# Kernel tuning notes

Hardware: AMD Instinct MI355X
Metric: run time of the kernel (lower is better)

## Reference

```python
import jax, jax.numpy as jnp
import numpy as np

MAX_REL = 128  # max_relative_position


def setup_inputs() -> dict:
    key = jax.random.key(0)
    k1, k2, k3, k4 = jax.random.split(key, 4)
    B, H, S, D = 2, 8, 2048, 64
    q = jax.random.normal(k1, (B, H, S, D), dtype=jnp.float32)
    k = jax.random.normal(k2, (B, H, S, D), dtype=jnp.float32)
    v = jax.random.normal(k3, (B, H, S, D), dtype=jnp.float32)
    rel_table = jax.random.normal(k4, (2 * MAX_REL + 1, D), dtype=jnp.float32)
    return {"q": q, "k": k, "v": v, "rel_table": rel_table}


def reference(q, k, v, rel_table):
    B, H, S, D = q.shape
    scale = jnp.sqrt(jnp.asarray(D, q.dtype))
    # content scores: [B,H,S,S]
    qk_scores = jnp.einsum('bhqd,bhkd->bhqk', q, k)
    # relative position index matrix [S,S] clamped to [-MAX_REL, MAX_REL]
    pos = jnp.arange(S)
    rel_idx = jnp.clip(pos[None, :] - pos[:, None], -MAX_REL, MAX_REL) + MAX_REL
    rel_emb = rel_table[rel_idx]  # [S,S,D]
    # relative scores: per-query dot with rel embedding row -> [B,H,S,S]
    rel_scores = jnp.einsum('bhqd,qkd->bhqk', q, rel_emb)
    scores = (qk_scores + rel_scores) / scale
    attn = jax.nn.softmax(scores, axis=-1)
    # output: [B,H,S,D]
    return jnp.einsum('bhqk,bhkd->bhqd', attn, v)
```

## Files before the change

### kernel.cpp

```cpp
#include <hip/hip_runtime.h>

typedef _Float16 half8 __attribute__((ext_vector_type(8)));
typedef _Float16 half4 __attribute__((ext_vector_type(4)));
typedef float f32x4 __attribute__((ext_vector_type(4)));

#define S_LEN 2048
#define HDIM 64
#define QBLK 64
#define KVBLK 64
#define NT (S_LEN / KVBLK)
#define QRS 258
#define NBH 16
#define L2E 1.44269504f
#define TSTR 72

__device__ __forceinline__ void load_lds16(const void* g, void* l) {
    __builtin_amdgcn_global_load_lds(
        (const __attribute__((address_space(1))) unsigned int*)g,
        (__attribute__((address_space(3))) unsigned int*)l, 16, 0, 0);
}

__global__ __launch_bounds__(256)
void convert_kv_kernel(const float* __restrict__ Kg, const float* __restrict__ Vg,
                       _Float16* __restrict__ Kh, _Float16* __restrict__ Vp)
{
    __shared__ _Float16 tile[KVBLK * TSTR];
    const int bid = blockIdx.x;
    const int tid = threadIdx.x;
    if (bid < 1024) {
        const int id = bid * 256 + tid;
        const int r  = id >> 3;
        const int d0 = (id & 7) * 8;
        const float* src = Kg + (size_t)r * HDIM + d0;
        f32x4 f0 = *(const f32x4*)(src);
        f32x4 f1 = *(const f32x4*)(src + 4);
        half8 h;
#pragma unroll
        for (int j = 0; j < 4; ++j) { h[j] = (_Float16)f0[j]; h[j+4] = (_Float16)f1[j]; }
        const int bh = r >> 11, kvg = r & 2047;
        const int t = kvg >> 6, kv = kvg & 63;
        const size_t blk = (size_t)(bh * NT + t) * 8192;
        const int off = (kv * 128 + d0 * 2) ^ ((kv & 7) << 4);
        *(half8*)((char*)Kh + blk + off) = h;
    } else {
        const int bt = bid - 1024;
        const int bh = bt >> 5, t = bt & 31;
        {
            const int kv = tid >> 2;
            const int d0 = (tid & 3) * 16;
            const float* src = Vg + ((size_t)bh * S_LEN + t * KVBLK + kv) * HDIM + d0;
            f32x4 f0 = *(const f32x4*)(src);
            f32x4 f1 = *(const f32x4*)(src + 4);
            f32x4 f2 = *(const f32x4*)(src + 8);
            f32x4 f3 = *(const f32x4*)(src + 12);
            half8 h0, h1;
#pragma unroll
            for (int j = 0; j < 4; ++j) {
                h0[j] = (_Float16)f0[j]; h0[j+4] = (_Float16)f1[j];
                h1[j] = (_Float16)f2[j]; h1[j+4] = (_Float16)f3[j];
            }
            *(half8*)&tile[kv * TSTR + d0]     = h0;
            *(half8*)&tile[kv * TSTR + d0 + 8] = h1;
        }
        __syncthreads();
        {
            const int dp = tid >> 2;
            const int u0 = (tid & 3) * 2;
            char* base = (char*)Vp + (size_t)bt * 8192;
            const int dsw = (dp & 7) << 4;
#pragma unroll
            for (int ui = 0; ui < 2; ++ui) {
                const int u  = u0 + ui;
                const int kc = u >> 2, gg = u & 3;
                half8 ch;
#pragma unroll
                for (int r = 0; r < 4; ++r) {
                    ch[r]     = tile[(32*kc + 4*gg + r)      * TSTR + dp];
                    ch[4 + r] = tile[(32*kc + 16 + 4*gg + r) * TSTR + dp];
                }
                *(half8*)(base + ((dp * 128 + u * 16) ^ dsw)) = ch;
            }
        }
    }
}

__global__ __launch_bounds__(512, 4)
void relattn_v7(const float* __restrict__ Qg, const float* __restrict__ RELg,
                const _Float16* __restrict__ Kh, const _Float16* __restrict__ Vp,
                float* __restrict__ Og)
{
    __shared__ __attribute__((aligned(16))) _Float16 Kbuf[2][4096];
    __shared__ __attribute__((aligned(16))) _Float16 Vbuf[2][4096];
    __shared__ __attribute__((aligned(16))) _Float16 Qrel[QBLK * QRS];
    __shared__ float MLds[2][64];
    __shared__ float LLds[2][64];

    const int tid  = threadIdx.x;
    const int wave = tid >> 6;
    const int lane = tid & 63;
    const int c  = lane & 15;
    const int g  = lane >> 4;
    const int qs = wave & 3;
    const int ks = wave >> 2;

    const int wk = ((blockIdx.x & 7) << 6) + (blockIdx.x >> 3);
    const int bh = wk >> 5;
    const int q0 = (wk & 31) * QBLK;
    const size_t hoff = (size_t)bh * S_LEN * HDIM;

    const int qb0 = q0 + 16 * qs;
    half8 bq[2];
#pragma unroll
    for (int kc = 0; kc < 2; ++kc) {
        const float* src = Qg + hoff + (size_t)(qb0 + c) * HDIM + kc * 32 + g * 8;
        f32x4 f0 = *(const f32x4*)(src);
        f32x4 f1 = *(const f32x4*)(src + 4);
        half8 h;
#pragma unroll
        for (int j = 0; j < 4; ++j) {
            h[j]     = (_Float16)(f0[j] * 0.125f);
            h[j + 4] = (_Float16)(f1[j] * 0.125f);
        }
        bq[kc] = h;
    }

    if (ks == 0) {
#pragma unroll 1
        for (int t = 0; t < 17; ++t) {
            f32x4 acc = {0.f, 0.f, 0.f, 0.f};
            int r = t * 16 + c;
            if (r > 256) r = 256;
#pragma unroll
            for (int kc = 0; kc < 2; ++kc) {
                const float* src = RELg + (size_t)r * HDIM + kc * 32 + g * 8;
                f32x4 f0 = *(const f32x4*)(src);
                f32x4 f1 = *(const f32x4*)(src + 4);
                half8 b;
#pragma unroll
                for (int j = 0; j < 4; ++j) { b[j] = (_Float16)f0[j]; b[j+4] = (_Float16)f1[j]; }
                acc = __builtin_amdgcn_mfma_f32_16x16x32_f16(bq[kc], b, acc, 0, 0, 0);
            }
            const int col = t * 16 + c;
            if (col <= 256) {
#pragma unroll
                for (int reg = 0; reg < 4; ++reg)
                    Qrel[(16 * qs + 4 * g + reg) * QRS + col] = (_Float16)acc[reg];
            }
        }
    }

    const char* kimg = (const char*)Kh + (size_t)bh * NT * 8192;
    const char* vimg = (const char*)Vp + (size_t)bh * NT * 8192;
    load_lds16(kimg + tid * 16, (char*)Kbuf + tid * 16);
    load_lds16(vimg + tid * 16, (char*)Vbuf + tid * 16);

    __syncthreads();

    const _Float16* qr = &Qrel[(16 * qs + c) * QRS];
    const float bias_lo = (float)qr[0];
    const float bias_hi = (float)qr[256];

    const int swz = (c & 7) << 4;
    int akoff[2][2], voff[4];
#pragma unroll
    for (int n = 0; n < 2; ++n)
#pragma unroll
        for (int kc = 0; kc < 2; ++kc)
            akoff[n][kc] = (((32 * ks + 16 * n + c) * 128) + kc * 64 + g * 16) ^ swz;
#pragma unroll
    for (int dn = 0; dn < 4; ++dn)
        voff[dn] = (((16 * dn + c) * 128) + ks * 64 + g * 16) ^ swz;

    half8 ones;
#pragma unroll
    for (int j = 0; j < 8; ++j) ones[j] = (_Float16)1.0f;

    float m = -1e30f;
    f32x4 l_acc = {0.f, 0.f, 0.f, 0.f};
    f32x4 oacc[4];
#pragma unroll
    for (int i = 0; i < 4; ++i) oacc[i] = (f32x4){0.f, 0.f, 0.f, 0.f};

#define BODY(t, b) do {                                                              \
        asm volatile("s_waitcnt vmcnt(0)" ::: "memory");                             \
        __builtin_amdgcn_s_barrier();                                                \
        {                                                                            \
            const int tn = ((t) + 1 < NT) ? (t) + 1 : (t);                           \
            load_lds16(kimg + (size_t)tn * 8192 + tid * 16,                          \
                       (char*)Kbuf + ((b) ^ 1) * 8192 + tid * 16);                   \
            load_lds16(vimg + (size_t)tn * 8192 + tid * 16,                          \
                       (char*)Vbuf + ((b) ^ 1) * 8192 + tid * 16);                   \
        }                                                                            \
        const char* kb = (const char*)Kbuf + (b) * 8192;                             \
        const char* vb = (const char*)Vbuf + (b) * 8192;                             \
        const int kws = (t) * KVBLK + 32 * ks;                                       \
        half8 a00 = *(const half8*)(kb + akoff[0][0]);                               \
        half8 a01 = *(const half8*)(kb + akoff[0][1]);                               \
        half8 a10 = *(const half8*)(kb + akoff[1][0]);                               \
        half8 a11 = *(const half8*)(kb + akoff[1][1]);                               \
        f32x4 s0 = {0.f,0.f,0.f,0.f}, s1 = {0.f,0.f,0.f,0.f};                        \
        __builtin_amdgcn_s_setprio(1);                                               \
        s0 = __builtin_amdgcn_mfma_f32_16x16x32_f16(a00, bq[0], s0, 0, 0, 0);        \
        s1 = __builtin_amdgcn_mfma_f32_16x16x32_f16(a10, bq[0], s1, 0, 0, 0);        \
        s0 = __builtin_amdgcn_mfma_f32_16x16x32_f16(a01, bq[1], s0, 0, 0, 0);        \
        s1 = __builtin_amdgcn_mfma_f32_16x16x32_f16(a11, bq[1], s1, 0, 0, 0);        \
        __builtin_amdgcn_s_setprio(0);                                               \
        float bias = 0.f;                                                            \
        float lm;                                                                    \
        if (kws + 159 <= qb0) {                                                      \
            bias = bias_lo;                                                          \
            lm = fmaxf(fmaxf(fmaxf(s0[0], s0[1]), fmaxf(s0[2], s0[3])),              \
                       fmaxf(fmaxf(s1[0], s1[1]), fmaxf(s1[2], s1[3]))) + bias;      \
        } else if (kws >= qb0 + 143) {                                               \
            bias = bias_hi;                                                          \
            lm = fmaxf(fmaxf(fmaxf(s0[0], s0[1]), fmaxf(s0[2], s0[3])),              \
                       fmaxf(fmaxf(s1[0], s1[1]), fmaxf(s1[2], s1[3]))) + bias;      \
        } else {                                                                     \
            const int base_d = kws + 4 * g - (qb0 + c) + 128;                        \
            _Pragma("unroll")                                                        \
            for (int r = 0; r < 4; ++r) {                                            \
                int i0 = base_d + r;                                                 \
                i0 = i0 < 0 ? 0 : (i0 > 256 ? 256 : i0);                             \
                int i1 = base_d + 16 + r;                                            \
                i1 = i1 < 0 ? 0 : (i1 > 256 ? 256 : i1);                             \
                s0[r] += (float)qr[i0];                                              \
                s1[r] += (float)qr[i1];                                              \
            }                                                                        \
            lm = fmaxf(fmaxf(fmaxf(s0[0], s0[1]), fmaxf(s0[2], s0[3])),              \
                       fmaxf(fmaxf(s1[0], s1[1]), fmaxf(s1[2], s1[3])));             \
        }                                                                            \
        if (!__all(lm <= m + 8.f)) {                                                 \
            float mt = lm;                                                           \
            mt = fmaxf(mt, __shfl_xor(mt, 16, 64));                                  \
            mt = fmaxf(mt, __shfl_xor(mt, 32, 64));                                  \
            const float mnew = fmaxf(m, mt);                                         \
            const float al = __builtin_amdgcn_exp2f((m - mnew) * L2E);               \
            m = mnew;                                                                \
            _Pragma("unroll")                                                        \
            for (int r = 0; r < 4; ++r) {                                            \
                const float ar = __shfl(al, 20 * g + r, 64);                         \
                l_acc[r] *= ar;                                                      \
                _Pragma("unroll")                                                    \
                for (int dn = 0; dn < 4; ++dn) oacc[dn][r] *= ar;                    \
            }                                                                        \
        }                                                                            \
        const float fold = (bias - m) * L2E;                                         \
        half8 ap;                                                                    \
        _Pragma("unroll")                                                            \
        for (int r = 0; r < 4; ++r) {                                                \
            ap[r]     = (_Float16)__builtin_amdgcn_exp2f(fmaf(s0[r], L2E, fold));    \
            ap[4 + r] = (_Float16)__builtin_amdgcn_exp2f(fmaf(s1[r], L2E, fold));    \
        }                                                                            \
        half8 v0 = *(const half8*)(vb + voff[0]);                                    \
        half8 v1 = *(const half8*)(vb + voff[1]);                                    \
        half8 v2 = *(const half8*)(vb + voff[2]);                                    \
        half8 v3 = *(const half8*)(vb + voff[3]);                                    \
        __builtin_amdgcn_s_setprio(1);                                               \
        l_acc   = __builtin_amdgcn_mfma_f32_16x16x32_f16(ap, ones, l_acc, 0, 0, 0);  \
        oacc[0] = __builtin_amdgcn_mfma_f32_16x16x32_f16(ap, v0, oacc[0], 0, 0, 0);  \
        oacc[1] = __builtin_amdgcn_mfma_f32_16x16x32_f16(ap, v1, oacc[1], 0, 0, 0);  \
        oacc[2] = __builtin_amdgcn_mfma_f32_16x16x32_f16(ap, v2, oacc[2], 0, 0, 0);  \
        oacc[3] = __builtin_amdgcn_mfma_f32_16x16x32_f16(ap, v3, oacc[3], 0, 0, 0);  \
        __builtin_amdgcn_s_setprio(0);                                               \
    } while (0)

#pragma unroll 1
    for (int tt = 0; tt < NT; tt += 2) {
        BODY(tt, 0);
        BODY(tt + 1, 1);
    }
#undef BODY

    asm volatile("s_waitcnt vmcnt(0)" ::: "memory");
    __syncthreads();

    {
        char* Ob = (char*)Kbuf;
#pragma unroll
        for (int r = 0; r < 4; ++r) {
            const int row = 16 * qs + 4 * g + r;
            const int rsw = (row & 7) << 4;
#pragma unroll
            for (int dn = 0; dn < 4; ++dn)
                *(_Float16*)(Ob + ks * 8192 + ((row * 128 + (16 * dn + c) * 2) ^ rsw))
                    = (_Float16)oacc[dn][r];
        }
        if (g == 0) MLds[ks][16 * qs + c] = m;
        if (c == 0) {
#pragma unroll
            for (int r = 0; r < 4; ++r)
                LLds[ks][16 * qs + 4 * g + r] = l_acc[r];
        }
        __syncthreads();

        const int row = 16 * qs + c;
        const int rsw = (c & 7) << 4;
        const float m0 = MLds[0][row], m1 = MLds[1][row];
        const float l0 = LLds[0][row], l1 = LLds[1][row];
        const float M  = fmaxf(m0, m1);
        const float w0 = __builtin_amdgcn_exp2f((m0 - M) * L2E);
        const float w1 = __builtin_amdgcn_exp2f((m1 - M) * L2E);
        const float inv = 1.0f / (l0 * w0 + l1 * w1);

        const int dof = 64 * ks + 16 * g;
        half8 o0 = *(const half8*)(Ob +        ((row * 128 + dof) ^ rsw));
        half8 o1 = *(const half8*)(Ob + 8192 + ((row * 128 + dof) ^ rsw));
        float* dst = Og + hoff + (size_t)(q0 + row) * HDIM + 32 * ks + 8 * g;
        f32x4 oA, oB;
#pragma unroll
        for (int j = 0; j < 4; ++j) {
            oA[j] = ((float)o0[j]     * w0 + (float)o1[j]     * w1) * inv;
            oB[j] = ((float)o0[4 + j] * w0 + (float)o1[4 + j] * w1) * inv;
        }
        *(f32x4*)dst = oA;
        *(f32x4*)(dst + 4) = oB;
    }
}

__global__ __launch_bounds__(256, 2)
void relattn_v1(const float* __restrict__ Qg, const float* __restrict__ Kg,
                const float* __restrict__ Vg, const float* __restrict__ RELg,
                float* __restrict__ Og)
{
    __shared__ _Float16 Klds[KVBLK * HDIM];
    __shared__ _Float16 Vt[HDIM * KVBLK];
    __shared__ _Float16 Plds[4][16 * KVBLK];
    __shared__ _Float16 Qrel[QBLK * QRS];

    const int tid  = threadIdx.x;
    const int wave = tid >> 6;
    const int lane = tid & 63;
    const int c = lane & 15;
    const int g = lane >> 4;

    const int bid = blockIdx.x;
    const int bh  = bid >> 5;
    const int q0  = (bid & 31) * QBLK;

    const size_t hoff = (size_t)bh * S_LEN * HDIM;
    const float* Qh = Qg + hoff;
    const float* Kh = Kg + hoff;
    const float* Vh = Vg + hoff;

    const int qrow_frag = q0 + wave * 16 + c;
    half8 aq[2];
#pragma unroll
    for (int kc = 0; kc < 2; ++kc) {
        const float* src = Qh + (size_t)qrow_frag * HDIM + kc * 32 + g * 8;
        f32x4 f0 = *(const f32x4*)(src);
        f32x4 f1 = *(const f32x4*)(src + 4);
        half8 h;
#pragma unroll
        for (int j = 0; j < 4; ++j) {
            h[j]     = (_Float16)(f0[j] * 0.125f);
            h[j + 4] = (_Float16)(f1[j] * 0.125f);
        }
        aq[kc] = h;
    }

#pragma unroll 1
    for (int t = 0; t < 17; ++t) {
        f32x4 acc = {0.f, 0.f, 0.f, 0.f};
        int r = t * 16 + c;
        if (r > 256) r = 256;
#pragma unroll
        for (int kc = 0; kc < 2; ++kc) {
            const float* src = RELg + (size_t)r * HDIM + kc * 32 + g * 8;
            f32x4 f0 = *(const f32x4*)(src);
            f32x4 f1 = *(const f32x4*)(src + 4);
            half8 b;
#pragma unroll
            for (int j = 0; j < 4; ++j) { b[j] = (_Float16)f0[j]; b[j+4] = (_Float16)f1[j]; }
            acc = __builtin_amdgcn_mfma_f32_16x16x32_f16(aq[kc], b, acc, 0, 0, 0);
        }
        const int col = t * 16 + c;
        if (col <= 256) {
#pragma unroll
            for (int reg = 0; reg < 4; ++reg)
                Qrel[(wave * 16 + 4 * g + reg) * QRS + col] = (_Float16)acc[reg];
        }
    }

    float mrow[4], lrow[4];
    f32x4 oacc[4];
#pragma unroll
    for (int i = 0; i < 4; ++i) {
        mrow[i] = -1e30f; lrow[i] = 0.f;
        oacc[i] = (f32x4){0.f, 0.f, 0.f, 0.f};
    }

    for (int k0 = 0; k0 < S_LEN; k0 += KVBLK) {
        __syncthreads();
        {
            const int r  = tid >> 2;
            const int dq = (tid & 3) << 4;
            const float* src = Kh + (size_t)(k0 + r) * HDIM + dq;
            f32x4 f0 = *(const f32x4*)(src);
            f32x4 f1 = *(const f32x4*)(src + 4);
            f32x4 f2 = *(const f32x4*)(src + 8);
            f32x4 f3 = *(const f32x4*)(src + 12);
            half8 h0, h1;
#pragma unroll
            for (int j = 0; j < 4; ++j) {
                h0[j] = (_Float16)f0[j]; h0[j+4] = (_Float16)f1[j];
                h1[j] = (_Float16)f2[j]; h1[j+4] = (_Float16)f3[j];
            }
            const int swz = (r & 7) << 4;
            char* base = (char*)Klds;
            *(half8*)(base + ((r * 128 + dq * 2) ^ swz))      = h0;
            *(half8*)(base + ((r * 128 + dq * 2 + 16) ^ swz)) = h1;
        }
        {
            const int kv = tid & 63;
            const int dbase = (tid >> 6) << 4;
            const float* src = Vh + (size_t)(k0 + kv) * HDIM + dbase;
            f32x4 f0 = *(const f32x4*)(src);
            f32x4 f1 = *(const f32x4*)(src + 4);
            f32x4 f2 = *(const f32x4*)(src + 8);
            f32x4 f3 = *(const f32x4*)(src + 12);
            float vals[16];
#pragma unroll
            for (int j = 0; j < 4; ++j) {
                vals[j] = f0[j]; vals[4+j] = f1[j]; vals[8+j] = f2[j]; vals[12+j] = f3[j];
            }
            char* base = (char*)Vt;
#pragma unroll
            for (int i = 0; i < 16; ++i) {
                const int d = dbase + i;
                const int off = (d * 128 + kv * 2) ^ ((d & 7) << 4);
                *(_Float16*)(base + off) = (_Float16)vals[i];
            }
        }
        __syncthreads();

        f32x4 sacc[4];
#pragma unroll
        for (int n = 0; n < 4; ++n) sacc[n] = (f32x4){0.f,0.f,0.f,0.f};
#pragma unroll
        for (int kc = 0; kc < 2; ++kc) {
#pragma unroll
            for (int n = 0; n < 4; ++n) {
                const int off = (((16*n + c) * 128) + kc * 64 + g * 16) ^ ((c & 7) << 4);
                half8 bk = *(const half8*)((const char*)Klds + off);
                sacc[n] = __builtin_amdgcn_mfma_f32_16x16x32_f16(aq[kc], bk, sacc[n], 0, 0, 0);
            }
        }

        float sval[4][4];
        const int myq0 = q0 + wave * 16 + 4 * g;
#pragma unroll
        for (int n = 0; n < 4; ++n) {
            const int kpos = k0 + 16 * n + c;
#pragma unroll
            for (int reg = 0; reg < 4; ++reg) {
                int rel = kpos - (myq0 + reg);
                rel = rel < -128 ? -128 : (rel > 128 ? 128 : rel);
                const float bias = (float)Qrel[(wave*16 + 4*g + reg) * QRS + (rel + 128)];
                sval[n][reg] = sacc[n][reg] + bias;
            }
        }

        float mt[4];
#pragma unroll
        for (int reg = 0; reg < 4; ++reg) {
            float mp = fmaxf(fmaxf(sval[0][reg], sval[1][reg]),
                             fmaxf(sval[2][reg], sval[3][reg]));
#pragma unroll
            for (int msk = 1; msk < 16; msk <<= 1)
                mp = fmaxf(mp, __shfl_xor(mp, msk, 64));
            mt[reg] = mp;
        }

        float alpha[4], psum[4];
#pragma unroll
        for (int reg = 0; reg < 4; ++reg) {
            const float mn = fmaxf(mrow[reg], mt[reg]);
            alpha[reg] = __expf(mrow[reg] - mn);
            mrow[reg] = mn;
            psum[reg] = 0.f;
        }

        char* pbase = (char*)&Plds[wave][0];
#pragma unroll
        for (int n = 0; n < 4; ++n) {
#pragma unroll
            for (int reg = 0; reg < 4; ++reg) {
                const float pv = __expf(sval[n][reg] - mrow[reg]);
                psum[reg] += pv;
                const int row = 4 * g + reg;
                const int off = (row * 128 + (16 * n + c) * 2) ^ ((row & 7) << 4);
                *(_Float16*)(pbase + off) = (_Float16)pv;
            }
        }

#pragma unroll
        for (int reg = 0; reg < 4; ++reg) {
            float ps = psum[reg];
#pragma unroll
            for (int msk = 1; msk < 16; msk <<= 1)
                ps += __shfl_xor(ps, msk, 64);
            lrow[reg] = lrow[reg] * alpha[reg] + ps;
#pragma unroll
            for (int dn = 0; dn < 4; ++dn) oacc[dn][reg] *= alpha[reg];
        }

        asm volatile("s_waitcnt lgkmcnt(0)" ::: "memory");

        half8 ap[2];
#pragma unroll
        for (int kc = 0; kc < 2; ++kc) {
            const int off = (c * 128 + kc * 64 + g * 16) ^ ((c & 7) << 4);
            ap[kc] = *(const half8*)(pbase + off);
        }
#pragma unroll
        for (int kc = 0; kc < 2; ++kc) {
#pragma unroll
            for (int dn = 0; dn < 4; ++dn) {
                const int drow = 16 * dn + c;
                const int off = (drow * 128 + kc * 64 + g * 16) ^ ((c & 7) << 4);
                half8 bv = *(const half8*)((const char*)Vt + off);
                oacc[dn] = __builtin_amdgcn_mfma_f32_16x16x32_f16(ap[kc], bv, oacc[dn], 0, 0, 0);
            }
        }
    }

#pragma unroll
    for (int reg = 0; reg < 4; ++reg) {
        const float inv = 1.0f / lrow[reg];
        const int row = q0 + wave * 16 + 4 * g + reg;
        float* dst = Og + hoff + (size_t)row * HDIM + c;
#pragma unroll
        for (int dn = 0; dn < 4; ++dn)
            dst[16 * dn] = oacc[dn][reg] * inv;
    }
}

extern "C" void kernel_launch(void* const* d_in, const int* in_sizes, int n_in,
                              void* d_out, int out_size, void* d_ws, size_t ws_size,
                              hipStream_t stream) {
    const float* q   = (const float*)d_in[0];
    const float* k   = (const float*)d_in[1];
    const float* v   = (const float*)d_in[2];
    const float* rel = (const float*)d_in[3];
    float* out = (float*)d_out;
    (void)in_sizes; (void)n_in; (void)out_size;

    const size_t kv_bytes = (size_t)NBH * S_LEN * HDIM * sizeof(_Float16);
    if (ws_size >= 2 * kv_bytes) {
        _Float16* KhB = (_Float16*)d_ws;
        _Float16* VpB = (_Float16*)((char*)d_ws + kv_bytes);
        convert_kv_kernel<<<dim3(1536), 256, 0, stream>>>(k, v, KhB, VpB);
        relattn_v7<<<dim3(NBH * (S_LEN / QBLK)), 512, 0, stream>>>(q, rel, KhB, VpB, out);
    } else {
        relattn_v1<<<dim3(NBH * (S_LEN / QBLK)), 256, 0, stream>>>(q, k, v, rel, out);
    }
}
```

Measured before the change: 58.59 us.

## Triple-buffer K tiles with staggered prefetch and hoist initial loads before Qrel

K tiles now use three LDS buffers and are prefetched two tiles ahead, while V stays double-buffered one tile ahead. The wait drops from vmcnt(0) to vmcnt(1), so the next K load can stay in flight while the current tile is processed. The first V tile and two K tiles are issued before the Q load and Qrel computation, so their latency overlaps that setup work. In exchange, LDS use grows by 8 KB per block, which may lower occupancy, and the buffer rotation across six unrolled bodies is more complex and easier to get wrong.

```diff
diff --git a/kernel.cpp b/kernel.cpp
--- a/kernel.cpp
+++ b/kernel.cpp
@@ -85,11 +85,11 @@
 }
 
 __global__ __launch_bounds__(512, 4)
-void relattn_v7(const float* __restrict__ Qg, const float* __restrict__ RELg,
+void relattn_v8(const float* __restrict__ Qg, const float* __restrict__ RELg,
                 const _Float16* __restrict__ Kh, const _Float16* __restrict__ Vp,
                 float* __restrict__ Og)
 {
-    __shared__ __attribute__((aligned(16))) _Float16 Kbuf[2][4096];
+    __shared__ __attribute__((aligned(16))) _Float16 Kbuf[3][4096];
     __shared__ __attribute__((aligned(16))) _Float16 Vbuf[2][4096];
     __shared__ __attribute__((aligned(16))) _Float16 Qrel[QBLK * QRS];
     __shared__ float MLds[2][64];
@@ -108,6 +108,13 @@
     const int q0 = (wk & 31) * QBLK;
     const size_t hoff = (size_t)bh * S_LEN * HDIM;
 
+    const char* kimg = (const char*)Kh + (size_t)bh * NT * 8192;
+    const char* vimg = (const char*)Vp + (size_t)bh * NT * 8192;
+
+    load_lds16(vimg + tid * 16, (char*)Vbuf + tid * 16);
+    load_lds16(kimg + tid * 16, (char*)Kbuf + tid * 16);
+    load_lds16(kimg + 8192 + tid * 16, (char*)&Kbuf[1][0] + tid * 16);
+
     const int qb0 = q0 + 16 * qs;
     half8 bq[2];
 #pragma unroll
@@ -148,12 +155,6 @@
             }
         }
     }
-
-    const char* kimg = (const char*)Kh + (size_t)bh * NT * 8192;
-    const char* vimg = (const char*)Vp + (size_t)bh * NT * 8192;
-    load_lds16(kimg + tid * 16, (char*)Kbuf + tid * 16);
-    load_lds16(vimg + tid * 16, (char*)Vbuf + tid * 16);
-
     __syncthreads();
 
     const _Float16* qr = &Qrel[(16 * qs + c) * QRS];
@@ -181,18 +182,19 @@
 #pragma unroll
     for (int i = 0; i < 4; ++i) oacc[i] = (f32x4){0.f, 0.f, 0.f, 0.f};
 
-#define BODY(t, b) do {                                                              \
-        asm volatile("s_waitcnt vmcnt(0)" ::: "memory");                             \
+#define BODY(t, KB, VB, VBN, KBN) do {                                               \
+        asm volatile("s_waitcnt vmcnt(1)" ::: "memory");                             \
         __builtin_amdgcn_s_barrier();                                                \
         {                                                                            \
-            const int tn = ((t) + 1 < NT) ? (t) + 1 : (t);                           \
-            load_lds16(kimg + (size_t)tn * 8192 + tid * 16,                          \
-                       (char*)Kbuf + ((b) ^ 1) * 8192 + tid * 16);                   \
-            load_lds16(vimg + (size_t)tn * 8192 + tid * 16,                          \
-                       (char*)Vbuf + ((b) ^ 1) * 8192 + tid * 16);                   \
+            const int tv = ((t) + 1 < NT) ? (t) + 1 : NT - 1;                        \
+            const int tk = ((t) + 2 < NT) ? (t) + 2 : NT - 1;                        \
+            load_lds16(vimg + (size_t)tv * 8192 + tid * 16,                          \
+                       (char*)&Vbuf[VBN][0] + tid * 16);                             \
+            load_lds16(kimg + (size_t)tk * 8192 + tid * 16,                          \
+                       (char*)&Kbuf[KBN][0] + tid * 16);                             \
         }                                                                            \
-        const char* kb = (const char*)Kbuf + (b) * 8192;                             \
-        const char* vb = (const char*)Vbuf + (b) * 8192;                             \
+        const char* kb = (const char*)&Kbuf[KB][0];                                  \
+        const char* vb = (const char*)&Vbuf[VB][0];                                  \
         const int kws = (t) * KVBLK + 32 * ks;                                       \
         half8 a00 = *(const half8*)(kb + akoff[0][0]);                               \
         half8 a01 = *(const half8*)(kb + akoff[0][1]);                               \
@@ -265,10 +267,16 @@
     } while (0)
 
 #pragma unroll 1
-    for (int tt = 0; tt < NT; tt += 2) {
-        BODY(tt, 0);
-        BODY(tt + 1, 1);
-    }
+    for (int tt = 0; tt < 30; tt += 6) {
+        BODY(tt + 0, 0, 0, 1, 2);
+        BODY(tt + 1, 1, 1, 0, 0);
+        BODY(tt + 2, 2, 0, 1, 1);
+        BODY(tt + 3, 0, 1, 0, 2);
+        BODY(tt + 4, 1, 0, 1, 0);
+        BODY(tt + 5, 2, 1, 0, 1);
+    }
+    BODY(30, 0, 0, 1, 2);
+    BODY(31, 1, 1, 0, 0);
 #undef BODY
 
     asm volatile("s_waitcnt vmcnt(0)" ::: "memory");
@@ -550,7 +558,7 @@
         _Float16* KhB = (_Float16*)d_ws;
         _Float16* VpB = (_Float16*)((char*)d_ws + kv_bytes);
         convert_kv_kernel<<<dim3(1536), 256, 0, stream>>>(k, v, KhB, VpB);
-        relattn_v7<<<dim3(NBH * (S_LEN / QBLK)), 512, 0, stream>>>(q, rel, KhB, VpB, out);
+        relattn_v8<<<dim3(NBH * (S_LEN / QBLK)), 512, 0, stream>>>(q, rel, KhB, VpB, out);
     } else {
         relattn_v1<<<dim3(NBH * (S_LEN / QBLK)), 256, 0, stream>>>(q, k, v, rel, out);
     }
```

After: 58.96 us. No clear change (+0.6%).

## Split attention into off-band and band kernels with partial-softmax merge

Applied to the files above, without the earlier changes.

Replaces the single fused attention kernel with two kernels. The first processes KV tiles far from the diagonal, split in two halves per query tile, using constant clamped bias values computed with a per-row dot product instead of the full Qrel table, and writes fp16 partial outputs plus max and sum to workspace. The second handles the up-to-five near-diagonal tiles with the full relative table and merges the partials. This removes the per-block 17-step Qrel precompute and the branching from the main loop and doubles the block count for better occupancy. The cost is an extra launch, extra workspace traffic and an fp16 rounding of the partial outputs.

```diff
diff --git a/kernel.cpp b/kernel.cpp
--- a/kernel.cpp
+++ b/kernel.cpp
@@ -6,9 +6,7 @@
 
 #define S_LEN 2048
 #define HDIM 64
-#define QBLK 64
-#define KVBLK 64
-#define NT (S_LEN / KVBLK)
+#define NT (S_LEN / 64)
 #define QRS 258
 #define NBH 16
 #define L2E 1.44269504f
@@ -24,7 +22,7 @@
 void convert_kv_kernel(const float* __restrict__ Kg, const float* __restrict__ Vg,
                        _Float16* __restrict__ Kh, _Float16* __restrict__ Vp)
 {
-    __shared__ _Float16 tile[KVBLK * TSTR];
+    __shared__ _Float16 tile[64 * TSTR];
     const int bid = blockIdx.x;
     const int tid = threadIdx.x;
     if (bid < 1024) {
@@ -48,7 +46,7 @@
         {
             const int kv = tid >> 2;
             const int d0 = (tid & 3) * 16;
-            const float* src = Vg + ((size_t)bh * S_LEN + t * KVBLK + kv) * HDIM + d0;
+            const float* src = Vg + ((size_t)bh * S_LEN + t * 64 + kv) * HDIM + d0;
             f32x4 f0 = *(const f32x4*)(src);
             f32x4 f1 = *(const f32x4*)(src + 4);
             f32x4 f2 = *(const f32x4*)(src + 8);
@@ -84,14 +82,14 @@
     }
 }
 
-__global__ __launch_bounds__(512, 4)
-void relattn_v7(const float* __restrict__ Qg, const float* __restrict__ RELg,
-                const _Float16* __restrict__ Kh, const _Float16* __restrict__ Vp,
-                float* __restrict__ Og)
+__global__ __launch_bounds__(512, 6)
+void offband_kernel(const float* __restrict__ Qg, const float* __restrict__ RELg,
+                    const _Float16* __restrict__ Kh, const _Float16* __restrict__ Vp,
+                    _Float16* __restrict__ Opart, float* __restrict__ Mpart,
+                    float* __restrict__ Lpart)
 {
     __shared__ __attribute__((aligned(16))) _Float16 Kbuf[2][4096];
     __shared__ __attribute__((aligned(16))) _Float16 Vbuf[2][4096];
-    __shared__ __attribute__((aligned(16))) _Float16 Qrel[QBLK * QRS];
     __shared__ float MLds[2][64];
     __shared__ float LLds[2][64];
 
@@ -103,62 +101,58 @@
     const int qs = wave & 3;
     const int ks = wave >> 2;
 
-    const int wk = ((blockIdx.x & 7) << 6) + (blockIdx.x >> 3);
-    const int bh = wk >> 5;
-    const int q0 = (wk & 31) * QBLK;
+    const int wk = ((blockIdx.x & 7) << 7) + (blockIdx.x >> 3);
+    const int qt = wk >> 1;
+    const int h  = wk & 1;
+    const int bh = qt >> 5, tq = qt & 31;
+    const int q0 = tq * 64;
     const size_t hoff = (size_t)bh * S_LEN * HDIM;
+
+    const int bt_lo = tq - 2 < 0 ? 0 : tq - 2;
+    const int bt_hi = tq + 2 > 31 ? 31 : tq + 2;
+    const int h0 = 16 * h;
+    const int s_ = h0 > bt_lo ? h0 : bt_lo;
+    const int e_ = (h0 + 15 < bt_hi) ? h0 + 15 : bt_hi;
+    int soff, L, N;
+    if (s_ > e_) { soff = 16; L = 0; N = 16; }
+    else         { soff = s_ - h0; L = e_ - s_ + 1; N = 16 - L; }
+
+    const char* kimg = (const char*)Kh + (size_t)bh * NT * 8192;
+    const char* vimg = (const char*)Vp + (size_t)bh * NT * 8192;
+
+    {
+        const int t0 = h0 + (0 >= soff ? L : 0);
+        load_lds16(kimg + (size_t)t0 * 8192 + tid * 16, (char*)&Kbuf[0][0] + tid * 16);
+        load_lds16(vimg + (size_t)t0 * 8192 + tid * 16, (char*)&Vbuf[0][0] + tid * 16);
+    }
 
     const int qb0 = q0 + 16 * qs;
     half8 bq[2];
+    float d_lo = 0.f, d_hi = 0.f;
 #pragma unroll
     for (int kc = 0; kc < 2; ++kc) {
-        const float* src = Qg + hoff + (size_t)(qb0 + c) * HDIM + kc * 32 + g * 8;
-        f32x4 f0 = *(const f32x4*)(src);
-        f32x4 f1 = *(const f32x4*)(src + 4);
-        half8 h;
+        const int dbase = kc * 32 + g * 8;
+        const float* qsrc = Qg + hoff + (size_t)(qb0 + c) * HDIM + dbase;
+        f32x4 f0 = *(const f32x4*)(qsrc);
+        f32x4 f1 = *(const f32x4*)(qsrc + 4);
+        f32x4 r0a = *(const f32x4*)(RELg + dbase);
+        f32x4 r0b = *(const f32x4*)(RELg + dbase + 4);
+        f32x4 r2a = *(const f32x4*)(RELg + 256 * HDIM + dbase);
+        f32x4 r2b = *(const f32x4*)(RELg + 256 * HDIM + dbase + 4);
+        half8 hq;
 #pragma unroll
         for (int j = 0; j < 4; ++j) {
-            h[j]     = (_Float16)(f0[j] * 0.125f);
-            h[j + 4] = (_Float16)(f1[j] * 0.125f);
-        }
-        bq[kc] = h;
-    }
-
-    if (ks == 0) {
-#pragma unroll 1
-        for (int t = 0; t < 17; ++t) {
-            f32x4 acc = {0.f, 0.f, 0.f, 0.f};
-            int r = t * 16 + c;
-            if (r > 256) r = 256;
-#pragma unroll
-            for (int kc = 0; kc < 2; ++kc) {
-                const float* src = RELg + (size_t)r * HDIM + kc * 32 + g * 8;
-                f32x4 f0 = *(const f32x4*)(src);
-                f32x4 f1 = *(const f32x4*)(src + 4);
-                half8 b;
-#pragma unroll
-                for (int j = 0; j < 4; ++j) { b[j] = (_Float16)f0[j]; b[j+4] = (_Float16)f1[j]; }
-                acc = __builtin_amdgcn_mfma_f32_16x16x32_f16(bq[kc], b, acc, 0, 0, 0);
-            }
-            const int col = t * 16 + c;
-            if (col <= 256) {
-#pragma unroll
-                for (int reg = 0; reg < 4; ++reg)
-                    Qrel[(16 * qs + 4 * g + reg) * QRS + col] = (_Float16)acc[reg];
-            }
-        }
-    }
-
-    const char* kimg = (const char*)Kh + (size_t)bh * NT * 8192;
-    const char* vimg = (const char*)Vp + (size_t)bh * NT * 8192;
-    load_lds16(kimg + tid * 16, (char*)Kbuf + tid * 16);
-    load_lds16(vimg + tid * 16, (char*)Vbuf + tid * 16);
-
-    __syncthreads();
-
-    const _Float16* qr = &Qrel[(16 * qs + c) * QRS];
-    const float bias_lo = (float)qr[0];
-    const float bias_hi = (float)qr[256];
+            hq[j]     = (_Float16)(f0[j] * 0.125f);
+            hq[j + 4] = (_Float16)(f1[j] * 0.125f);
+            d_lo += f0[j] * r0a[j] + f1[j] * r0b[j];
+            d_hi += f0[j] * r2a[j] + f1[j] * r2b[j];
+        }
+        bq[kc] = hq;
+    }
+    d_lo += __shfl_xor(d_lo, 16, 64); d_lo += __shfl_xor(d_lo, 32, 64);
+    d_hi += __shfl_xor(d_hi, 16, 64); d_hi += __shfl_xor(d_hi, 32, 64);
+    const float bias_lo = d_lo * 0.125f;
+    const float bias_hi = d_hi * 0.125f;
 
     const int swz = (c & 7) << 4;
     int akoff[2][2], voff[4];
@@ -181,99 +175,72 @@
 #pragma unroll
     for (int i = 0; i < 4; ++i) oacc[i] = (f32x4){0.f, 0.f, 0.f, 0.f};
 
-#define BODY(t, b) do {                                                              \
-        asm volatile("s_waitcnt vmcnt(0)" ::: "memory");                             \
-        __builtin_amdgcn_s_barrier();                                                \
-        {                                                                            \
-            const int tn = ((t) + 1 < NT) ? (t) + 1 : (t);                           \
-            load_lds16(kimg + (size_t)tn * 8192 + tid * 16,                          \
-                       (char*)Kbuf + ((b) ^ 1) * 8192 + tid * 16);                   \
-            load_lds16(vimg + (size_t)tn * 8192 + tid * 16,                          \
-                       (char*)Vbuf + ((b) ^ 1) * 8192 + tid * 16);                   \
-        }                                                                            \
-        const char* kb = (const char*)Kbuf + (b) * 8192;                             \
-        const char* vb = (const char*)Vbuf + (b) * 8192;                             \
-        const int kws = (t) * KVBLK + 32 * ks;                                       \
-        half8 a00 = *(const half8*)(kb + akoff[0][0]);                               \
-        half8 a01 = *(const half8*)(kb + akoff[0][1]);                               \
-        half8 a10 = *(const half8*)(kb + akoff[1][0]);                               \
-        half8 a11 = *(const half8*)(kb + akoff[1][1]);                               \
-        f32x4 s0 = {0.f,0.f,0.f,0.f}, s1 = {0.f,0.f,0.f,0.f};                        \
-        __builtin_amdgcn_s_setprio(1);                                               \
-        s0 = __builtin_amdgcn_mfma_f32_16x16x32_f16(a00, bq[0], s0, 0, 0, 0);        \
-        s1 = __builtin_amdgcn_mfma_f32_16x16x32_f16(a10, bq[0], s1, 0, 0, 0);        \
-        s0 = __builtin_amdgcn_mfma_f32_16x16x32_f16(a01, bq[1], s0, 0, 0, 0);        \
-        s1 = __builtin_amdgcn_mfma_f32_16x16x32_f16(a11, bq[1], s1, 0, 0, 0);        \
-        __builtin_amdgcn_s_setprio(0);                                               \
-        float bias = 0.f;                                                            \
-        float lm;                                                                    \
-        if (kws + 159 <= qb0) {                                                      \
-            bias = bias_lo;                                                          \
-            lm = fmaxf(fmaxf(fmaxf(s0[0], s0[1]), fmaxf(s0[2], s0[3])),              \
-                       fmaxf(fmaxf(s1[0], s1[1]), fmaxf(s1[2], s1[3]))) + bias;      \
-        } else if (kws >= qb0 + 143) {                                               \
-            bias = bias_hi;                                                          \
-            lm = fmaxf(fmaxf(fmaxf(s0[0], s0[1]), fmaxf(s0[2], s0[3])),              \
-                       fmaxf(fmaxf(s1[0], s1[1]), fmaxf(s1[2], s1[3]))) + bias;      \
-        } else {                                                                     \
-            const int base_d = kws + 4 * g - (qb0 + c) + 128;                        \
-            _Pragma("unroll")                                                        \
-            for (int r = 0; r < 4; ++r) {                                            \
-                int i0 = base_d + r;                                                 \
-                i0 = i0 < 0 ? 0 : (i0 > 256 ? 256 : i0);                             \
-                int i1 = base_d + 16 + r;                                            \
-                i1 = i1 < 0 ? 0 : (i1 > 256 ? 256 : i1);                             \
-                s0[r] += (float)qr[i0];                                              \
-                s1[r] += (float)qr[i1];                                              \
-            }                                                                        \
-            lm = fmaxf(fmaxf(fmaxf(s0[0], s0[1]), fmaxf(s0[2], s0[3])),              \
-                       fmaxf(fmaxf(s1[0], s1[1]), fmaxf(s1[2], s1[3])));             \
-        }                                                                            \
-        if (!__all(lm <= m + 8.f)) {                                                 \
-            float mt = lm;                                                           \
-            mt = fmaxf(mt, __shfl_xor(mt, 16, 64));                                  \
-            mt = fmaxf(mt, __shfl_xor(mt, 32, 64));                                  \
-            const float mnew = fmaxf(m, mt);                                         \
-            const float al = __builtin_amdgcn_exp2f((m - mnew) * L2E);               \
-            m = mnew;                                                                \
-            _Pragma("unroll")                                                        \
-            for (int r = 0; r < 4; ++r) {                                            \
-                const float ar = __shfl(al, 20 * g + r, 64);                         \
-                l_acc[r] *= ar;                                                      \
-                _Pragma("unroll")                                                    \
-                for (int dn = 0; dn < 4; ++dn) oacc[dn][r] *= ar;                    \
-            }                                                                        \
-        }                                                                            \
-        const float fold = (bias - m) * L2E;                                         \
-        half8 ap;                                                                    \
-        _Pragma("unroll")                                                            \
-        for (int r = 0; r < 4; ++r) {                                                \
-            ap[r]     = (_Float16)__builtin_amdgcn_exp2f(fmaf(s0[r], L2E, fold));    \
-            ap[4 + r] = (_Float16)__builtin_amdgcn_exp2f(fmaf(s1[r], L2E, fold));    \
-        }                                                                            \
-        half8 v0 = *(const half8*)(vb + voff[0]);                                    \
-        half8 v1 = *(const half8*)(vb + voff[1]);                                    \
-        half8 v2 = *(const half8*)(vb + voff[2]);                                    \
-        half8 v3 = *(const half8*)(vb + voff[3]);                                    \
-        __builtin_amdgcn_s_setprio(1);                                               \
-        l_acc   = __builtin_amdgcn_mfma_f32_16x16x32_f16(ap, ones, l_acc, 0, 0, 0);  \
-        oacc[0] = __builtin_amdgcn_mfma_f32_16x16x32_f16(ap, v0, oacc[0], 0, 0, 0);  \
-        oacc[1] = __builtin_amdgcn_mfma_f32_16x16x32_f16(ap, v1, oacc[1], 0, 0, 0);  \
-        oacc[2] = __builtin_amdgcn_mfma_f32_16x16x32_f16(ap, v2, oacc[2], 0, 0, 0);  \
-        oacc[3] = __builtin_amdgcn_mfma_f32_16x16x32_f16(ap, v3, oacc[3], 0, 0, 0);  \
-        __builtin_amdgcn_s_setprio(0);                                               \
-    } while (0)
-
 #pragma unroll 1
-    for (int tt = 0; tt < NT; tt += 2) {
-        BODY(tt, 0);
-        BODY(tt + 1, 1);
-    }
-#undef BODY
+    for (int i = 0; i < N; ++i) {
+        const int b = i & 1;
+        asm volatile("s_waitcnt vmcnt(0)" ::: "memory");
+        __builtin_amdgcn_s_barrier();
+        if (i + 1 < N) {
+            const int tn = h0 + i + 1 + (i + 1 >= soff ? L : 0);
+            load_lds16(kimg + (size_t)tn * 8192 + tid * 16, (char*)&Kbuf[b ^ 1][0] + tid * 16);
+            load_lds16(vimg + (size_t)tn * 8192 + tid * 16, (char*)&Vbuf[b ^ 1][0] + tid * 16);
+        }
+        const int t = h0 + i + (i >= soff ? L : 0);
+        const char* kb = (const char*)&Kbuf[b][0];
+        const char* vb = (const char*)&Vbuf[b][0];
+
+        half8 a00 = *(const half8*)(kb + akoff[0][0]);
+        half8 a01 = *(const half8*)(kb + akoff[0][1]);
+        half8 a10 = *(const half8*)(kb + akoff[1][0]);
+        half8 a11 = *(const half8*)(kb + akoff[1][1]);
+        f32x4 s0 = {0.f,0.f,0.f,0.f}, s1 = {0.f,0.f,0.f,0.f};
+        __builtin_amdgcn_s_setprio(1);
+        s0 = __builtin_amdgcn_mfma_f32_16x16x32_f16(a00, bq[0], s0, 0, 0, 0);
+        s1 = __builtin_amdgcn_mfma_f32_16x16x32_f16(a10, bq[0], s1, 0, 0, 0);
+        s0 = __builtin_amdgcn_mfma_f32_16x16x32_f16(a01, bq[1], s0, 0, 0, 0);
+        s1 = __builtin_amdgcn_mfma_f32_16x16x32_f16(a11, bq[1], s1, 0, 0, 0);
+        __builtin_amdgcn_s_setprio(0);
+
+        const float bias = (t < tq) ? bias_lo : bias_hi;
+        float lm = fmaxf(fmaxf(fmaxf(s0[0], s0[1]), fmaxf(s0[2], s0[3])),
+                         fmaxf(fmaxf(s1[0], s1[1]), fmaxf(s1[2], s1[3]))) + bias;
+        if (!__all(lm <= m + 8.f)) {
+            float mt = lm;
+            mt = fmaxf(mt, __shfl_xor(mt, 16, 64));
+            mt = fmaxf(mt, __shfl_xor(mt, 32, 64));
+            const float mnew = fmaxf(m, mt);
+            const float al = __builtin_amdgcn_exp2f((m - mnew) * L2E);
+            m = mnew;
+#pragma unroll
+            for (int r = 0; r < 4; ++r) {
+                const float ar = __shfl(al, 20 * g + r, 64);
+                l_acc[r] *= ar;
+#pragma unroll
+                for (int dn = 0; dn < 4; ++dn) oacc[dn][r] *= ar;
+            }
+        }
+        const float fold = (bias - m) * L2E;
+        half8 ap;
+#pragma unroll
+        for (int r = 0; r < 4; ++r) {
+            ap[r]     = (_Float16)__builtin_amdgcn_exp2f(fmaf(s0[r], L2E, fold));
+            ap[4 + r] = (_Float16)__builtin_amdgcn_exp2f(fmaf(s1[r], L2E, fold));
+        }
+        half8 v0 = *(const half8*)(vb + voff[0]);
+        half8 v1 = *(const half8*)(vb + voff[1]);
+        half8 v2 = *(const half8*)(vb + voff[2]);
+        half8 v3 = *(const half8*)(vb + voff[3]);
+        __builtin_amdgcn_s_setprio(1);
+        l_acc   = __builtin_amdgcn_mfma_f32_16x16x32_f16(ap, ones, l_acc, 0, 0, 0);
+        oacc[0] = __builtin_amdgcn_mfma_f32_16x16x32_f16(ap, v0, oacc[0], 0, 0, 0);
+        oacc[1] = __builtin_amdgcn_mfma_f32_16x16x32_f16(ap, v1, oacc[1], 0, 0, 0);
+        oacc[2] = __builtin_amdgcn_mfma_f32_16x16x32_f16(ap, v2, oacc[2], 0, 0, 0);
+        oacc[3] = __builtin_amdgcn_mfma_f32_16x16x32_f16(ap, v3, oacc[3], 0, 0, 0);
+        __builtin_amdgcn_s_setprio(0);
+    }
 
     asm volatile("s_waitcnt vmcnt(0)" ::: "memory");
     __syncthreads();
-
     {
         char* Ob = (char*)Kbuf;
 #pragma unroll
@@ -300,17 +267,249 @@
         const float M  = fmaxf(m0, m1);
         const float w0 = __builtin_amdgcn_exp2f((m0 - M) * L2E);
         const float w1 = __builtin_amdgcn_exp2f((m1 - M) * L2E);
-        const float inv = 1.0f / (l0 * w0 + l1 * w1);
+        const float den = l0 * w0 + l1 * w1;
+        const float S8 = __builtin_amdgcn_exp2f(-8.0f * L2E);
 
         const int dof = 64 * ks + 16 * g;
         half8 o0 = *(const half8*)(Ob +        ((row * 128 + dof) ^ rsw));
         half8 o1 = *(const half8*)(Ob + 8192 + ((row * 128 + dof) ^ rsw));
+        half8 ow;
+#pragma unroll
+        for (int j = 0; j < 8; ++j)
+            ow[j] = (_Float16)(((float)o0[j] * w0 + (float)o1[j] * w1) * S8);
+        *(half8*)(Opart + (size_t)(qt * 2 + h) * 4096 + row * 64 + 32 * ks + 8 * g) = ow;
+        if (ks == 0 && g == 0) {
+            Mpart[(size_t)(qt * 2 + h) * 64 + row] = M + 8.0f;
+            Lpart[(size_t)(qt * 2 + h) * 64 + row] = den * S8;
+        }
+    }
+}
+
+__global__ __launch_bounds__(512, 4)
+void band_kernel(const float* __restrict__ Qg, const float* __restrict__ RELg,
+                 const _Float16* __restrict__ Kh, const _Float16* __restrict__ Vp,
+                 const _Float16* __restrict__ Opart, const float* __restrict__ Mpart,
+                 const float* __restrict__ Lpart, float* __restrict__ Og)
+{
+    __shared__ __attribute__((aligned(16))) _Float16 Kbuf[2][4096];
+    __shared__ __attribute__((aligned(16))) _Float16 Vbuf[2][4096];
+    __shared__ __attribute__((aligned(16))) _Float16 Qrel[64 * QRS];
+    __shared__ float MLds[2][64];
+    __shared__ float LLds[2][64];
+
+    const int tid  = threadIdx.x;
+    const int wave = tid >> 6;
+    const int lane = tid & 63;
+    const int c  = lane & 15;
+    const int g  = lane >> 4;
+    const int qs = wave & 3;
+    const int ks = wave >> 2;
+
+    const int qt = ((blockIdx.x & 7) << 6) + (blockIdx.x >> 3);
+    const int bh = qt >> 5, tq = qt & 31;
+    const int q0 = tq * 64;
+    const size_t hoff = (size_t)bh * S_LEN * HDIM;
+
+    const int bt_lo = tq - 2 < 0 ? 0 : tq - 2;
+    const int bt_hi = tq + 2 > 31 ? 31 : tq + 2;
+    const int NB = bt_hi - bt_lo + 1;
+
+    const char* kimg = (const char*)Kh + (size_t)bh * NT * 8192;
+    const char* vimg = (const char*)Vp + (size_t)bh * NT * 8192;
+
+    load_lds16(kimg + (size_t)bt_lo * 8192 + tid * 16, (char*)&Kbuf[0][0] + tid * 16);
+    load_lds16(vimg + (size_t)bt_lo * 8192 + tid * 16, (char*)&Vbuf[0][0] + tid * 16);
+
+    const int qb0 = q0 + 16 * qs;
+    half8 bq[2];
+#pragma unroll
+    for (int kc = 0; kc < 2; ++kc) {
+        const float* src = Qg + hoff + (size_t)(qb0 + c) * HDIM + kc * 32 + g * 8;
+        f32x4 f0 = *(const f32x4*)(src);
+        f32x4 f1 = *(const f32x4*)(src + 4);
+        half8 hq;
+#pragma unroll
+        for (int j = 0; j < 4; ++j) {
+            hq[j]     = (_Float16)(f0[j] * 0.125f);
+            hq[j + 4] = (_Float16)(f1[j] * 0.125f);
+        }
+        bq[kc] = hq;
+    }
+
+    if (ks == 0) {
+#pragma unroll 1
+        for (int t = 0; t < 17; ++t) {
+            f32x4 acc = {0.f, 0.f, 0.f, 0.f};
+            int r = t * 16 + c;
+            if (r > 256) r = 256;
+#pragma unroll
+            for (int kc = 0; kc < 2; ++kc) {
+                const float* src = RELg + (size_t)r * HDIM + kc * 32 + g * 8;
+                f32x4 f0 = *(const f32x4*)(src);
+                f32x4 f1 = *(const f32x4*)(src + 4);
+                half8 b;
+#pragma unroll
+                for (int j = 0; j < 4; ++j) { b[j] = (_Float16)f0[j]; b[j+4] = (_Float16)f1[j]; }
+                acc = __builtin_amdgcn_mfma_f32_16x16x32_f16(bq[kc], b, acc, 0, 0, 0);
+            }
+            const int col = t * 16 + c;
+            if (col <= 256) {
+#pragma unroll
+                for (int reg = 0; reg < 4; ++reg)
+                    Qrel[(16 * qs + 4 * g + reg) * QRS + col] = (_Float16)acc[reg];
+            }
+        }
+    }
+    __syncthreads();
+    const _Float16* qr = &Qrel[(16 * qs + c) * QRS];
+
+    const int swz = (c & 7) << 4;
+    int akoff[2][2], voff[4];
+#pragma unroll
+    for (int n = 0; n < 2; ++n)
+#pragma unroll
+        for (int kc = 0; kc < 2; ++kc)
+            akoff[n][kc] = (((32 * ks + 16 * n + c) * 128) + kc * 64 + g * 16) ^ swz;
+#pragma unroll
+    for (int dn = 0; dn < 4; ++dn)
+        voff[dn] = (((16 * dn + c) * 128) + ks * 64 + g * 16) ^ swz;
+
+    half8 ones;
+#pragma unroll
+    for (int j = 0; j < 8; ++j) ones[j] = (_Float16)1.0f;
+
+    float m = -1e30f;
+    f32x4 l_acc = {0.f, 0.f, 0.f, 0.f};
+    f32x4 oacc[4];
+#pragma unroll
+    for (int i = 0; i < 4; ++i) oacc[i] = (f32x4){0.f, 0.f, 0.f, 0.f};
+
+#pragma unroll 1
+    for (int i = 0; i < NB; ++i) {
+        const int b = i & 1;
+        asm volatile("s_waitcnt vmcnt(0)" ::: "memory");
+        __builtin_amdgcn_s_barrier();
+        if (i + 1 < NB) {
+            const int tn = bt_lo + i + 1;
+            load_lds16(kimg + (size_t)tn * 8192 + tid * 16, (char*)&Kbuf[b ^ 1][0] + tid * 16);
+            load_lds16(vimg + (size_t)tn * 8192 + tid * 16, (char*)&Vbuf[b ^ 1][0] + tid * 16);
+        }
+        const int t = bt_lo + i;
+        const char* kb = (const char*)&Kbuf[b][0];
+        const char* vb = (const char*)&Vbuf[b][0];
+
+        half8 a00 = *(const half8*)(kb + akoff[0][0]);
+        half8 a01 = *(const half8*)(kb + akoff[0][1]);
+        half8 a10 = *(const half8*)(kb + akoff[1][0]);
+        half8 a11 = *(const half8*)(kb + akoff[1][1]);
+        f32x4 s0 = {0.f,0.f,0.f,0.f}, s1 = {0.f,0.f,0.f,0.f};
+        __builtin_amdgcn_s_setprio(1);
+        s0 = __builtin_amdgcn_mfma_f32_16x16x32_f16(a00, bq[0], s0, 0, 0, 0);
+        s1 = __builtin_amdgcn_mfma_f32_16x16x32_f16(a10, bq[0], s1, 0, 0, 0);
+        s0 = __builtin_amdgcn_mfma_f32_16x16x32_f16(a01, bq[1], s0, 0, 0, 0);
+        s1 = __builtin_amdgcn_mfma_f32_16x16x32_f16(a11, bq[1], s1, 0, 0, 0);
+        __builtin_amdgcn_s_setprio(0);
+
+        const int kws = t * 64 + 32 * ks;
+        const int base_d = kws + 4 * g - (qb0 + c) + 128;
+        float lm = -1e30f;
+#pragma unroll
+        for (int r = 0; r < 4; ++r) {
+            int i0 = base_d + r;
+            i0 = i0 < 0 ? 0 : (i0 > 256 ? 256 : i0);
+            int i1 = base_d + 16 + r;
+            i1 = i1 < 0 ? 0 : (i1 > 256 ? 256 : i1);
+            s0[r] += (float)qr[i0];
+            s1[r] += (float)qr[i1];
+            lm = fmaxf(lm, fmaxf(s0[r], s1[r]));
+        }
+        if (!__all(lm <= m + 8.f)) {
+            float mt = lm;
+            mt = fmaxf(mt, __shfl_xor(mt, 16, 64));
+            mt = fmaxf(mt, __shfl_xor(mt, 32, 64));
+            const float mnew = fmaxf(m, mt);
+            const float al = __builtin_amdgcn_exp2f((m - mnew) * L2E);
+            m = mnew;
+#pragma unroll
+            for (int r = 0; r < 4; ++r) {
+                const float ar = __shfl(al, 20 * g + r, 64);
+                l_acc[r] *= ar;
+#pragma unroll
+                for (int dn = 0; dn < 4; ++dn) oacc[dn][r] *= ar;
+            }
+        }
+        const float fold = -m * L2E;
+        half8 ap;
+#pragma unroll
+        for (int r = 0; r < 4; ++r) {
+            ap[r]     = (_Float16)__builtin_amdgcn_exp2f(fmaf(s0[r], L2E, fold));
+            ap[4 + r] = (_Float16)__builtin_amdgcn_exp2f(fmaf(s1[r], L2E, fold));
+        }
+        half8 v0 = *(const half8*)(vb + voff[0]);
+        half8 v1 = *(const half8*)(vb + voff[1]);
+        half8 v2 = *(const half8*)(vb + voff[2]);
+        half8 v3 = *(const half8*)(vb + voff[3]);
+        __builtin_amdgcn_s_setprio(1);
+        l_acc   = __builtin_amdgcn_mfma_f32_16x16x32_f16(ap, ones, l_acc, 0, 0, 0);
+        oacc[0] = __builtin_amdgcn_mfma_f32_16x16x32_f16(ap, v0, oacc[0], 0, 0, 0);
+        oacc[1] = __builtin_amdgcn_mfma_f32_16x16x32_f16(ap, v1, oacc[1], 0, 0, 0);
+        oacc[2] = __builtin_amdgcn_mfma_f32_16x16x32_f16(ap, v2, oacc[2], 0, 0, 0);
+        oacc[3] = __builtin_amdgcn_mfma_f32_16x16x32_f16(ap, v3, oacc[3], 0, 0, 0);
+        __builtin_amdgcn_s_setprio(0);
+    }
+
+    asm volatile("s_waitcnt vmcnt(0)" ::: "memory");
+    __syncthreads();
+    {
+        char* Ob = (char*)Kbuf;
+#pragma unroll
+        for (int r = 0; r < 4; ++r) {
+            const int row = 16 * qs + 4 * g + r;
+            const int rsw = (row & 7) << 4;
+#pragma unroll
+            for (int dn = 0; dn < 4; ++dn)
+                *(_Float16*)(Ob + ks * 8192 + ((row * 128 + (16 * dn + c) * 2) ^ rsw))
+                    = (_Float16)oacc[dn][r];
+        }
+        if (g == 0) MLds[ks][16 * qs + c] = m;
+        if (c == 0) {
+#pragma unroll
+            for (int r = 0; r < 4; ++r)
+                LLds[ks][16 * qs + 4 * g + r] = l_acc[r];
+        }
+        __syncthreads();
+
+        const int row = 16 * qs + c;
+        const int rsw = (c & 7) << 4;
+        const float mb0 = MLds[0][row], mb1 = MLds[1][row];
+        const float lb0 = LLds[0][row], lb1 = LLds[1][row];
+        const size_t pA = (size_t)(qt * 2 + 0) * 64 + row;
+        const size_t pB = (size_t)(qt * 2 + 1) * 64 + row;
+        const float moa = Mpart[pA], mob = Mpart[pB];
+        const float loa = Lpart[pA], lob = Lpart[pB];
+        const float M = fmaxf(fmaxf(mb0, mb1), fmaxf(moa, mob));
+        const float wb0 = __builtin_amdgcn_exp2f((mb0 - M) * L2E);
+        const float wb1 = __builtin_amdgcn_exp2f((mb1 - M) * L2E);
+        const float woa = __builtin_amdgcn_exp2f((moa - M) * L2E);
+        const float wob = __builtin_amdgcn_exp2f((mob - M) * L2E);
+        const float inv = 1.0f / (lb0 * wb0 + lb1 * wb1 + loa * woa + lob * wob);
+
+        const int dof = 64 * ks + 16 * g;
+        half8 o0 = *(const half8*)(Ob +        ((row * 128 + dof) ^ rsw));
+        half8 o1 = *(const half8*)(Ob + 8192 + ((row * 128 + dof) ^ rsw));
+        const _Float16* oa_p = Opart + (size_t)(qt * 2 + 0) * 4096 + row * 64 + 32 * ks + 8 * g;
+        const _Float16* ob_p = Opart + (size_t)(qt * 2 + 1) * 4096 + row * 64 + 32 * ks + 8 * g;
+        half8 oa = *(const half8*)oa_p;
+        half8 ob2 = *(const half8*)ob_p;
+
         float* dst = Og + hoff + (size_t)(q0 + row) * HDIM + 32 * ks + 8 * g;
         f32x4 oA, oB;
 #pragma unroll
         for (int j = 0; j < 4; ++j) {
-            oA[j] = ((float)o0[j]     * w0 + (float)o1[j]     * w1) * inv;
-            oB[j] = ((float)o0[4 + j] * w0 + (float)o1[4 + j] * w1) * inv;
+            oA[j] = ((float)o0[j]     * wb0 + (float)o1[j]     * wb1 +
+                     (float)oa[j]     * woa + (float)ob2[j]    * wob) * inv;
+            oB[j] = ((float)o0[4 + j] * wb0 + (float)o1[4 + j] * wb1 +
+                     (float)oa[4 + j] * woa + (float)ob2[4 + j] * wob) * inv;
         }
         *(f32x4*)dst = oA;
         *(f32x4*)(dst + 4) = oB;
@@ -322,10 +521,10 @@
                 const float* __restrict__ Vg, const float* __restrict__ RELg,
                 float* __restrict__ Og)
 {
-    __shared__ _Float16 Klds[KVBLK * HDIM];
-    __shared__ _Float16 Vt[HDIM * KVBLK];
-    __shared__ _Float16 Plds[4][16 * KVBLK];
-    __shared__ _Float16 Qrel[QBLK * QRS];
+    __shared__ _Float16 Klds[64 * HDIM];
+    __shared__ _Float16 Vt[HDIM * 64];
+    __shared__ _Float16 Plds[4][16 * 64];
+    __shared__ _Float16 Qrel[64 * QRS];
 
     const int tid  = threadIdx.x;
     const int wave = tid >> 6;
@@ -335,7 +534,7 @@
 
     const int bid = blockIdx.x;
     const int bh  = bid >> 5;
-    const int q0  = (bid & 31) * QBLK;
+    const int q0  = (bid & 31) * 64;
 
     const size_t hoff = (size_t)bh * S_LEN * HDIM;
     const float* Qh = Qg + hoff;
@@ -389,7 +588,7 @@
         oacc[i] = (f32x4){0.f, 0.f, 0.f, 0.f};
     }
 
-    for (int k0 = 0; k0 < S_LEN; k0 += KVBLK) {
+    for (int k0 = 0; k0 < S_LEN; k0 += 64) {
         __syncthreads();
         {
             const int r  = tid >> 2;
@@ -546,12 +745,21 @@
     (void)in_sizes; (void)n_in; (void)out_size;
 
     const size_t kv_bytes = (size_t)NBH * S_LEN * HDIM * sizeof(_Float16);
-    if (ws_size >= 2 * kv_bytes) {
-        _Float16* KhB = (_Float16*)d_ws;
-        _Float16* VpB = (_Float16*)((char*)d_ws + kv_bytes);
+    const size_t op_bytes = (size_t)1024 * 4096 * sizeof(_Float16);
+    const size_t ml_bytes = (size_t)1024 * 64 * sizeof(float);
+    const size_t need = 2 * kv_bytes + op_bytes + 2 * ml_bytes;
+
+    if (ws_size >= need) {
+        char* p = (char*)d_ws;
+        _Float16* KhB = (_Float16*)p;   p += kv_bytes;
+        _Float16* VpB = (_Float16*)p;   p += kv_bytes;
+        _Float16* OpB = (_Float16*)p;   p += op_bytes;
+        float*    MpB = (float*)p;      p += ml_bytes;
+        float*    LpB = (float*)p;
         convert_kv_kernel<<<dim3(1536), 256, 0, stream>>>(k, v, KhB, VpB);
-        relattn_v7<<<dim3(NBH * (S_LEN / QBLK)), 512, 0, stream>>>(q, rel, KhB, VpB, out);
+        offband_kernel<<<dim3(1024), 512, 0, stream>>>(q, rel, KhB, VpB, OpB, MpB, LpB);
+        band_kernel<<<dim3(512), 512, 0, stream>>>(q, rel, KhB, VpB, OpB, MpB, LpB, out);
     } else {
-        relattn_v1<<<dim3(NBH * (S_LEN / QBLK)), 256, 0, stream>>>(q, k, v, rel, out);
+        relattn_v1<<<dim3(512), 256, 0, stream>>>(q, k, v, rel, out);
     }
 }
```

New measurement: 71.18 us. 1.21x slower.
